# Kernel tuning notes

Measured on AMD Instinct MI355X. Metric: run time of the kernel, lower is better.

Reference implementation:

```python
import jax, jax.numpy as jnp
import numpy as np
from jax import lax
from jax.scipy.special import logsumexp

N = 1024   # keypoints image 0
M = 1024   # keypoints image 1
D = 256    # descriptor dim
H = 4      # attention heads
L = 18     # GNN layers ('self','cross')*9
ITERS = 100
KENC = [4, 32, 64, 128, 256]


def conv1(x, w, b):
    # 1x1 Conv1d == channel matmul: x [b,c,n], w [o,c], b [o]
    return jnp.einsum('oc,bcn->bon', w, x) + b[None, :, None]


def inorm(x, eps=1e-5):
    # InstanceNorm1d (affine=False): normalize over length per (b, c)
    m = jnp.mean(x, axis=-1, keepdims=True)
    v = jnp.var(x, axis=-1, keepdims=True)
    return (x - m) * lax.rsqrt(v + eps)


def attention_block(x, src, pw, pb, mw, mb):
    b, d, _ = x.shape
    dh = d // H
    q = conv1(x, pw[0], pb[0]).reshape(b, dh, H, -1)
    k = conv1(src, pw[1], pb[1]).reshape(b, dh, H, -1)
    v = conv1(src, pw[2], pb[2]).reshape(b, dh, H, -1)
    s = jnp.einsum('bdhn,bdhm->bhnm', q, k) / (dh ** 0.5)
    p = jax.nn.softmax(s, axis=-1)
    o = jnp.einsum('bhnm,bdhm->bdhn', p, v).reshape(b, d, -1)
    return conv1(o, mw, mb)


def prop(x, src, i, Pw, Pb, Mw, Mb, W0, B0, W1, B1):
    msg = attention_block(x, src, Pw[i], Pb[i], Mw[i], Mb[i])
    h = jnp.concatenate([x, msg], axis=1)          # [b, 2D, n]
    h = jax.nn.relu(inorm(conv1(h, W0[i], B0[i])))
    return conv1(h, W1[i], B1[i])


def sinkhorn(Z, log_mu, log_nu, iters):
    def step(carry, _):
        u, v = carry
        u = log_mu - logsumexp(Z + v[:, None, :], axis=2)
        v = log_nu - logsumexp(Z + u[:, :, None], axis=1)
        return (u, v), None
    init = (jnp.zeros_like(log_mu), jnp.zeros_like(log_nu))
    (u, v), _ = lax.scan(jax.checkpoint(step), init, None, length=iters)
    return Z + u[:, :, None] + v[:, None, :]


def log_optimal_transport(scores, alpha, iters):
    b, m, n = scores.shape
    bins0 = jnp.broadcast_to(alpha, (b, m, 1))
    bins1 = jnp.broadcast_to(alpha, (b, 1, n))
    binsA = jnp.broadcast_to(alpha, (b, 1, 1))
    couplings = jnp.concatenate([
        jnp.concatenate([scores, bins0], axis=-1),
        jnp.concatenate([bins1, binsA], axis=-1)], axis=1)  # [b, m+1, n+1]
    norm = np.float32(-np.log(m + n))
    log_mu = jnp.concatenate([jnp.full((m,), norm, scores.dtype),
                              jnp.array([np.log(n)], scores.dtype) + norm])
    log_nu = jnp.concatenate([jnp.full((n,), norm, scores.dtype),
                              jnp.array([np.log(m)], scores.dtype) + norm])
    log_mu = jnp.broadcast_to(log_mu[None], (b, m + 1))
    log_nu = jnp.broadcast_to(log_nu[None], (b, n + 1))
    Z = sinkhorn(couplings, log_mu, log_nu, iters)
    return Z - norm


def setup_inputs() -> dict:
    key = jax.random.key(0)
    ks = iter(jax.random.split(key, 64))
    w = lambda shape, s=0.02: jax.random.normal(next(ks), shape, jnp.float32) * s
    inp = {
        'keypoints0': jax.random.normal(next(ks), (1, N, 3), jnp.float32),
        'keypoints1': jax.random.normal(next(ks), (1, M, 3), jnp.float32),
        'descriptors0': jax.random.normal(next(ks), (1, D, N), jnp.float32),
        'descriptors1': jax.random.normal(next(ks), (1, D, M), jnp.float32),
        'scores0': jax.random.uniform(next(ks), (1, N), jnp.float32),
        'scores1': jax.random.uniform(next(ks), (1, M), jnp.float32),
    }
    for i in range(4):
        inp[f'kenc_w{i}'] = w((KENC[i + 1], KENC[i]), 0.1)
        inp[f'kenc_b{i}'] = jnp.zeros((KENC[i + 1],), jnp.float32)
    inp['gnn_proj_w'] = w((L, 3, D, D))
    inp['gnn_proj_b'] = jnp.zeros((L, 3, D), jnp.float32)
    inp['gnn_merge_w'] = w((L, D, D))
    inp['gnn_merge_b'] = jnp.zeros((L, D), jnp.float32)
    inp['gnn_mlp_w0'] = w((L, 2 * D, 2 * D))
    inp['gnn_mlp_b0'] = jnp.zeros((L, 2 * D), jnp.float32)
    inp['gnn_mlp_w1'] = w((L, D, 2 * D))
    inp['gnn_mlp_b1'] = jnp.zeros((L, D), jnp.float32)
    inp['final_w'] = w((D, D))
    inp['final_b'] = jnp.zeros((D,), jnp.float32)
    inp['bin_score'] = jnp.float32(1.0)
    return inp


def reference(keypoints0, keypoints1, descriptors0, descriptors1, scores0, scores1,
              kenc_w0, kenc_b0, kenc_w1, kenc_b1, kenc_w2, kenc_b2, kenc_w3, kenc_b3,
              gnn_proj_w, gnn_proj_b, gnn_merge_w, gnn_merge_b,
              gnn_mlp_w0, gnn_mlp_b0, gnn_mlp_w1, gnn_mlp_b1,
              final_w, final_b, bin_score):
    def kenc(kpts, sc):
        h = jnp.concatenate([jnp.swapaxes(kpts, 1, 2), sc[:, None, :]], axis=1)  # [b,4,n]
        h = jax.nn.relu(inorm(conv1(h, kenc_w0, kenc_b0)))
        h = jax.nn.relu(inorm(conv1(h, kenc_w1, kenc_b1)))
        h = jax.nn.relu(inorm(conv1(h, kenc_w2, kenc_b2)))
        return conv1(h, kenc_w3, kenc_b3)

    d0 = descriptors0 + kenc(keypoints0, scores0)
    d1 = descriptors1 + kenc(keypoints1, scores1)
    for i in range(L):  # even: self, odd: cross
        cross = (i % 2 == 1)
        s0 = d1 if cross else d0
        s1 = d0 if cross else d1
        delta0 = prop(d0, s0, i, gnn_proj_w, gnn_proj_b, gnn_merge_w, gnn_merge_b,
                      gnn_mlp_w0, gnn_mlp_b0, gnn_mlp_w1, gnn_mlp_b1)
        delta1 = prop(d1, s1, i, gnn_proj_w, gnn_proj_b, gnn_merge_w, gnn_merge_b,
                      gnn_mlp_w0, gnn_mlp_b0, gnn_mlp_w1, gnn_mlp_b1)
        d0, d1 = d0 + delta0, d1 + delta1
    md0 = conv1(d0, final_w, final_b)
    md1 = conv1(d1, final_w, final_b)
    scores = jnp.einsum('bdn,bdm->bnm', md0, md1) / (D ** 0.5)
    return log_optimal_transport(scores, bin_score, ITERS)
```

## Files before the change

### kernel.cpp

```cpp
#include <hip/hip_runtime.h>
#include <cstddef>

#define TPB 256

typedef _Float16 f16;
typedef _Float16 f16x4 __attribute__((ext_vector_type(4)));
typedef _Float16 f16x8 __attribute__((ext_vector_type(8)));
typedef float f32x4 __attribute__((ext_vector_type(4)));
typedef unsigned long long u64;

__device__ __forceinline__ float block_sum(float v, float* red) {
  int tid = threadIdx.x;
  red[tid] = v; __syncthreads();
#pragma unroll
  for (int off = 128; off > 0; off >>= 1) {
    if (tid < off) red[tid] += red[tid + off];
    __syncthreads();
  }
  float r = red[0];
  __syncthreads();
  return r;
}

__global__ __launch_bounds__(TPB) void build_h0(const float* __restrict__ kp0,
                                                const float* __restrict__ kp1,
                                                const float* __restrict__ sc0,
                                                const float* __restrict__ sc1,
                                                float* __restrict__ h0) {
  int n = blockIdx.x * TPB + threadIdx.x;
  int im = blockIdx.y;
  const float* kp = im ? kp1 : kp0;
  const float* sc = im ? sc1 : sc0;
  float* h = h0 + (size_t)im * 4096;
  h[n]        = kp[n * 3 + 0];
  h[1024 + n] = kp[n * 3 + 1];
  h[2048 + n] = kp[n * 3 + 2];
  h[3072 + n] = sc[n];
}

template<bool NORMRELU, bool RESID>
__global__ __launch_bounds__(TPB) void chanconv(const float* __restrict__ W,
                                                const float* __restrict__ bias,
                                                const float* __restrict__ in, long instride,
                                                const float* res0, const float* res1,
                                                float* __restrict__ out, long outstride, int C) {
  int o = blockIdx.x, im = blockIdx.y, tid = threadIdx.x;
  const float* inp = in + (long)im * instride;
  __shared__ float Ws[128];
  __shared__ float red[TPB];
  for (int c = tid; c < C; c += TPB) Ws[c] = W[(long)o * C + c];
  __syncthreads();
  float b = bias[o];
  float4 acc = {b, b, b, b};
  for (int c = 0; c < C; ++c) {
    float w = Ws[c];
    float4 v = *(const float4*)(inp + (long)c * 1024 + tid * 4);
    acc.x += w * v.x; acc.y += w * v.y; acc.z += w * v.z; acc.w += w * v.w;
  }
  float* orow = out + (long)im * outstride + (long)o * 1024;
  if (NORMRELU) {
    float s = acc.x + acc.y + acc.z + acc.w;
    float mean = block_sum(s, red) * (1.f / 1024.f);
    float dx = acc.x - mean, dy = acc.y - mean, dz = acc.z - mean, dw = acc.w - mean;
    float var = block_sum(dx * dx + dy * dy + dz * dz + dw * dw, red) * (1.f / 1024.f);
    float rstd = rsqrtf(var + 1e-5f);
    float4 o4 = {fmaxf(dx * rstd, 0.f), fmaxf(dy * rstd, 0.f),
                 fmaxf(dz * rstd, 0.f), fmaxf(dw * rstd, 0.f)};
    *(float4*)(orow + tid * 4) = o4;
  } else {
    if (RESID) {
      const float* res = im ? res1 : res0;
      float4 r = *(const float4*)(res + (long)o * 1024 + tid * 4);
      acc.x += r.x; acc.y += r.y; acc.z += r.z; acc.w += r.w;
    }
    *(float4*)(orow + tid * 4) = acc;
  }
}

struct GBH {
  const void* A; const void* B; const void* B2; void* C;
  const float* bias; const float* res; const float* mu; const float* rs;
  void* o2a; void* o2b; int coff; int pad;
};
struct GB16 { GBH g[16]; };

#define F_BNORM   1
#define F_BCONCAT 2
#define F_BADD    4
#define F_CD16    8
#define F_RES     16
#define F_OUT2    32
#define F_CSCAT   64

template<int BM, int BN, int ASRC, int BSRC, int FLAGS>
__global__ __launch_bounds__(TPB) void gemmh(GB16 gbs, int K, int lda, int ldb,
                                             int ldc, float alpha, int ksplit) {
  constexpr int WM = BM / 32;
  constexpr int NWN = 4 / WM;
  constexpr int WN = BN / NWN;
  constexpr int NFR = WN / 16;
  GBH g = gbs.g[blockIdx.z];
  const int tid = threadIdx.x;
  const int lane = tid & 63, wid = tid >> 6;
  const int wm = wid / NWN, wn = wid % NWN;
  const int m0 = blockIdx.y * BM, n0 = blockIdx.x * BN;
  __shared__ f16 As[BM][36];
  __shared__ f16 Bs[BN][36];
  f32x4 acc[2][NFR];
#pragma unroll
  for (int i = 0; i < 2; ++i)
#pragma unroll
    for (int j = 0; j < NFR; ++j) acc[i][j] = (f32x4){0.f, 0.f, 0.f, 0.f};

  for (int k0 = 0; k0 < K; k0 += 32) {
    if constexpr (ASRC == 0) {
      if constexpr (BM == 64) {
        const int m = tid >> 2, k4 = (tid & 3) * 8;
        const float* ap = (const float*)g.A + (long)(m0 + m) * lda + k0 + k4;
        float4 u0 = *(const float4*)ap, u1 = *(const float4*)(ap + 4);
        f16x4 h0 = {(f16)u0.x, (f16)u0.y, (f16)u0.z, (f16)u0.w};
        f16x4 h1 = {(f16)u1.x, (f16)u1.y, (f16)u1.z, (f16)u1.w};
        *(f16x4*)&As[m][k4] = h0;
        *(f16x4*)&As[m][k4 + 4] = h1;
      } else {
        const int m = tid >> 3, k4 = (tid & 7) * 4;
        const float* ap = (const float*)g.A + (long)(m0 + m) * lda + k0 + k4;
        float4 u0 = *(const float4*)ap;
        f16x4 h0 = {(f16)u0.x, (f16)u0.y, (f16)u0.z, (f16)u0.w};
        *(f16x4*)&As[m][k4] = h0;
      }
    } else if constexpr (ASRC == 1) {
      const int k = tid >> 3, mg = (tid & 7) * 8;
      const f16* ap = (const f16*)g.A + (long)(k0 + k) * lda + m0 + mg;
      f16x8 h = *(const f16x8*)ap;
#pragma unroll
      for (int j = 0; j < 8; ++j) As[mg + j][k] = h[j];
    } else {
      const int m = tid >> 2, k4 = (tid & 3) * 8;
      const f16* ap = (const f16*)g.A + (long)(m0 + m) * lda + k0 + k4;
      f16x8 h = *(const f16x8*)ap;
      const float M = g.mu[m0 + m], Iv = g.rs[m0 + m];
      f16x4 h0, h1;
#pragma unroll
      for (int j = 0; j < 4; ++j) h0[j] = (f16)(__expf((float)h[j] - M) * Iv);
#pragma unroll
      for (int j = 0; j < 4; ++j) h1[j] = (f16)(__expf((float)h[j + 4] - M) * Iv);
      *(f16x4*)&As[m][k4] = h0;
      *(f16x4*)&As[m][k4 + 4] = h1;
    }
#pragma unroll
    for (int r = 0; r < BN / 64; ++r) {
      if constexpr (BSRC == 0) {
        const int k = tid >> 3, ng = (tid & 7) * 8 + r * 64;
        const int kg = k0 + k;
        const float* bp;
        if constexpr ((FLAGS & F_BCONCAT) != 0)
          bp = (kg < ksplit) ? ((const float*)g.B + (long)kg * ldb)
                             : ((const float*)g.B2 + (long)(kg - ksplit) * ldb);
        else
          bp = (const float*)g.B + (long)kg * ldb;
        float4 u0 = *(const float4*)(bp + n0 + ng);
        float4 u1 = *(const float4*)(bp + n0 + ng + 4);
        Bs[ng + 0][k] = (f16)u0.x; Bs[ng + 1][k] = (f16)u0.y;
        Bs[ng + 2][k] = (f16)u0.z; Bs[ng + 3][k] = (f16)u0.w;
        Bs[ng + 4][k] = (f16)u1.x; Bs[ng + 5][k] = (f16)u1.y;
        Bs[ng + 6][k] = (f16)u1.z; Bs[ng + 7][k] = (f16)u1.w;
      } else if constexpr (BSRC == 1) {
        const int k = tid >> 3, ng = (tid & 7) * 8 + r * 64;
        const int kg = k0 + k;
        f16x8 h = *(const f16x8*)((const f16*)g.B + (long)kg * ldb + n0 + ng);
        if constexpr ((FLAGS & F_BNORM) != 0) {
          const float mu = g.mu[kg], rs = g.rs[kg];
#pragma unroll
          for (int j = 0; j < 8; ++j)
            h[j] = (f16)fmaxf(((float)h[j] - mu) * rs, 0.f);
        }
#pragma unroll
        for (int j = 0; j < 8; ++j) Bs[ng + j][k] = h[j];
      } else {
        const int n = (tid >> 2) + r * 64, k4 = (tid & 3) * 8;
        const f16* bp = (const f16*)g.B + (long)(n0 + n) * ldb + k0 + k4;
        f16x8 h = *(const f16x8*)bp;
        if constexpr ((FLAGS & F_BADD) != 0) {
          f16x8 h2 = *(const f16x8*)((const f16*)g.B2 + (long)(n0 + n) * ldb + k0 + k4);
          h = h + h2;
        }
        f16x4 h0 = {h[0], h[1], h[2], h[3]};
        f16x4 h1 = {h[4], h[5], h[6], h[7]};
        *(f16x4*)&Bs[n][k4] = h0;
        *(f16x4*)&Bs[n][k4 + 4] = h1;
      }
    }
    __syncthreads();
#pragma unroll
    for (int ks = 0; ks < 2; ++ks) {
      const int kof = ks * 16 + ((lane >> 4) << 2);
      f16x4 a[2], b[NFR];
      a[0] = *(const f16x4*)&As[wm * 32 + (lane & 15)][kof];
      a[1] = *(const f16x4*)&As[wm * 32 + 16 + (lane & 15)][kof];
#pragma unroll
      for (int fn = 0; fn < NFR; ++fn)
        b[fn] = *(const f16x4*)&Bs[wn * WN + fn * 16 + (lane & 15)][kof];
#pragma unroll
      for (int fm = 0; fm < 2; ++fm)
#pragma unroll
        for (int fn = 0; fn < NFR; ++fn)
          acc[fm][fn] = __builtin_amdgcn_mfma_f32_16x16x16f16(a[fm], b[fn], acc[fm][fn], 0, 0, 0);
    }
    __syncthreads();
  }

  const int r0 = (lane >> 4) << 2, cn = lane & 15;
#pragma unroll
  for (int fm = 0; fm < 2; ++fm) {
#pragma unroll
    for (int r = 0; r < 4; ++r) {
      const int m = m0 + wm * 32 + fm * 16 + r0 + r;
      const float bi = g.bias ? g.bias[m] : 0.f;
#pragma unroll
      for (int fn = 0; fn < NFR; ++fn) {
        const int n = n0 + wn * WN + fn * 16 + cn;
        float v = acc[fm][fn][r] * alpha + bi;
        if constexpr ((FLAGS & F_RES) != 0) v += g.res[(long)m * ldc + n];
        if constexpr ((FLAGS & F_OUT2) != 0) {
          ((float*)g.C)[(long)m * 1028 + n] = v;
          ((f16*)g.o2a)[(long)m * 1028 + n] = (f16)v;
          ((f16*)g.o2b)[(long)n * 1028 + m] = (f16)v;
        } else if constexpr ((FLAGS & F_CSCAT) != 0) {
          ((f16*)g.C)[(long)m * ldc + g.coff + 4 * n] = (f16)v;
        } else if constexpr ((FLAGS & F_CD16) != 0) {
          ((f16*)g.C)[(long)m * ldc + n] = (f16)v;
        } else {
          ((float*)g.C)[(long)m * ldc + n] = v;
        }
      }
    }
  }
}

__global__ __launch_bounds__(TPB) void rowlse_h(const f16* __restrict__ S,
                                                float* __restrict__ Mrow,
                                                float* __restrict__ Inv) {
  int row = blockIdx.x * 4 + (threadIdx.x >> 6);
  int lane = threadIdx.x & 63;
  const f16x8* p = (const f16x8*)(S + (long)row * 1024);
  f16x8 v0 = p[lane], v1 = p[lane + 64];
  float m = -1e30f;
#pragma unroll
  for (int j = 0; j < 8; ++j)
    m = fmaxf(m, fmaxf((float)v0[j], (float)v1[j]));
#pragma unroll
  for (int off = 32; off > 0; off >>= 1) m = fmaxf(m, __shfl_xor(m, off));
  float s = 0.f;
#pragma unroll
  for (int j = 0; j < 8; ++j)
    s += __expf((float)v0[j] - m) + __expf((float)v1[j] - m);
#pragma unroll
  for (int off = 32; off > 0; off >>= 1) s += __shfl_xor(s, off);
  if (lane == 0) { Mrow[row] = m; Inv[row] = 1.f / s; }
}

__global__ __launch_bounds__(TPB) void rowstats2_h(const f16* __restrict__ t,
                                                   float* __restrict__ mu,
                                                   float* __restrict__ rs) {
  int row = blockIdx.x * 4 + (threadIdx.x >> 6);
  int lane = threadIdx.x & 63;
  const f16x8* p = (const f16x8*)(t + (long)row * 1024);
  f16x8 v0 = p[lane], v1 = p[lane + 64];
  float s = 0.f, s2 = 0.f;
#pragma unroll
  for (int j = 0; j < 8; ++j) {
    float a = (float)v0[j], b = (float)v1[j];
    s += a + b; s2 += a * a + b * b;
  }
#pragma unroll
  for (int off = 32; off > 0; off >>= 1) { s += __shfl_xor(s, off); s2 += __shfl_xor(s2, off); }
  if (lane == 0) {
    float mean = s * (1.f / 1024.f);
    mu[row] = mean;
    rs[row] = rsqrtf(fmaxf(s2 * (1.f / 1024.f) - mean * mean, 0.f) + 1e-5f);
  }
}

#define NORMC  (-7.62461899f)
#define LOGN   (6.93147181f)
#define LOG_MN (7.62461899f)
#define ZLD    1028
#define SINKB  64

__device__ __forceinline__ u64 llc_load64(const u64* p) {
  return __hip_atomic_load(p, __ATOMIC_RELAXED, __HIP_MEMORY_SCOPE_AGENT);
}
__device__ __forceinline__ void llc_store64(u64* p, u64 v) {
  __hip_atomic_store(p, v, __ATOMIC_RELAXED, __HIP_MEMORY_SCOPE_AGENT);
}
__device__ __forceinline__ void llc_store32(float* p, float v) {
  __hip_atomic_store(p, v, __ATOMIC_RELAXED, __HIP_MEMORY_SCOPE_AGENT);
}
__device__ __forceinline__ u64 pack2(float a, float b) {
  union { float f[2]; u64 x; } c; c.f[0] = a; c.f[1] = b; return c.x;
}

__global__ __launch_bounds__(TPB) void fill_bins(float* __restrict__ Z,
                                                 const float* __restrict__ alpha_p,
                                                 float* __restrict__ vF,
                                                 unsigned* __restrict__ bar) {
  float a = *alpha_p;
  int t = blockIdx.x * TPB + threadIdx.x;
  if (t < ZLD) vF[t] = 0.f;
  if (t == 0) *bar = 0u;
  if (t <= 1024) {
    Z[(long)t * ZLD + 1024] = a;
    Z[(long)1024 * ZLD + t] = a;
  }
}

__device__ __forceinline__ void gridbar(unsigned* __restrict__ bar, unsigned gen) {
  __syncthreads();
  if (threadIdx.x == 0) {
    __hip_atomic_fetch_add(bar, 1u, __ATOMIC_RELAXED, __HIP_MEMORY_SCOPE_AGENT);
    const unsigned target = gen * SINKB;
    while (__hip_atomic_load(bar, __ATOMIC_RELAXED, __HIP_MEMORY_SCOPE_AGENT) < target) {}
  }
  asm volatile("" ::: "memory");
  __syncthreads();
}

__device__ __forceinline__ void sink_half(const f16x8 zreg[4][2],
                                          const float* __restrict__ w,
                                          float* __restrict__ out,
                                          int tid, int gw, int lane,
                                          float alpha, float* __restrict__ lds) {
  for (int s = tid; s < 513; s += TPB) {
    u64 x = llc_load64((const u64*)w + s);
    union { u64 x; float f[2]; } c; c.x = x;
    lds[2 * s] = c.f[0];
    lds[2 * s + 1] = c.f[1];
  }
  __syncthreads();
  float vv[16];
#pragma unroll
  for (int t = 0; t < 16; ++t) vv[t] = lds[lane + 64 * t];
  const float w1024 = lds[1024];
  const float binv = alpha + w1024;

  float res[4];
#pragma unroll
  for (int r = 0; r < 4; ++r) {
    float val[16];
    float m = binv;
#pragma unroll
    for (int t = 0; t < 16; ++t) {
      val[t] = (float)zreg[r][t >> 3][t & 7] + vv[t];
      m = fmaxf(m, val[t]);
    }
#pragma unroll
    for (int off = 32; off > 0; off >>= 1) m = fmaxf(m, __shfl_xor(m, off));
    float s = 0.f;
#pragma unroll
    for (int t = 0; t < 16; ++t) s += __expf(val[t] - m);
#pragma unroll
    for (int off = 32; off > 0; off >>= 1) s += __shfl_xor(s, off);
    s += __expf(binv - m);
    res[r] = NORMC - (m + logf(s));
  }
  if (lane < 2)
    llc_store64((u64*)(out + 4 * gw) + lane, pack2(res[2 * lane], res[2 * lane + 1]));

  if (gw == 0) {
    float m = w1024;
#pragma unroll
    for (int t = 0; t < 16; ++t) m = fmaxf(m, vv[t]);
#pragma unroll
    for (int off = 32; off > 0; off >>= 1) m = fmaxf(m, __shfl_xor(m, off));
    float s = 0.f;
#pragma unroll
    for (int t = 0; t < 16; ++t) s += __expf(vv[t] - m);
#pragma unroll
    for (int off = 32; off > 0; off >>= 1) s += __shfl_xor(s, off);
    s += __expf(w1024 - m);
    if (lane == 0)
      llc_store32(out + 1024, NORMC + LOGN - (alpha + m + logf(s)));
  }
}

__global__ __launch_bounds__(TPB) void sink_persist(const f16* __restrict__ Zh,
                                                    const f16* __restrict__ Zth,
                                                    float* __restrict__ uF,
                                                    float* __restrict__ vF,
                                                    unsigned* __restrict__ bar,
                                                    const float* __restrict__ alpha_p) {
  __shared__ float lds[ZLD];
  const int tid = threadIdx.x;
  const int lane = tid & 63;
  const int gw = blockIdx.x * 4 + (tid >> 6);
  const float alpha = *alpha_p;

  f16x8 zr[4][2], zt[4][2];
#pragma unroll
  for (int r = 0; r < 4; ++r) {
    const long row = 4 * gw + r;
    const f16* zp = Zh + row * ZLD;
    const f16* ztp = Zth + row * ZLD;
#pragma unroll
    for (int h = 0; h < 2; ++h)
#pragma unroll
      for (int j = 0; j < 8; ++j) {
        zr[r][h][j] = zp[lane + 64 * (8 * h + j)];
        zt[r][h][j] = ztp[lane + 64 * (8 * h + j)];
      }
  }

  unsigned gen = 0;
#pragma unroll 1
  for (int it = 0; it < 100; ++it) {
    sink_half(zr, vF, uF, tid, gw, lane, alpha, lds);
    gridbar(bar, ++gen);
    sink_half(zt, uF, vF, tid, gw, lane, alpha, lds);
    gridbar(bar, ++gen);
  }
}

__global__ __launch_bounds__(TPB) void assemble(const float* __restrict__ Z,
                                                const float* __restrict__ u,
                                                const float* __restrict__ v,
                                                float* __restrict__ out) {
  int idx = blockIdx.x * TPB + threadIdx.x;
  if (idx < 1025 * 1025) {
    int i = idx / 1025;
    int j = idx - i * 1025;
    out[idx] = Z[(long)i * ZLD + j] + u[i] + v[j] + LOG_MN;
  }
}

static inline GBH mkgb(const void* A, const void* B, void* C,
                       const float* bias = nullptr, const void* B2 = nullptr,
                       const float* res = nullptr,
                       const float* mu = nullptr, const float* rs = nullptr,
                       int coff = 0, void* o2a = nullptr, void* o2b = nullptr) {
  GBH g; g.A = A; g.B = B; g.B2 = B2; g.C = C; g.bias = bias; g.res = res;
  g.mu = mu; g.rs = rs; g.o2a = o2a; g.o2b = o2b; g.coff = coff; g.pad = 0;
  return g;
}

extern "C" void kernel_launch(void* const* d_in, const int* in_sizes, int n_in,
                              void* d_out, int out_size, void* d_ws, size_t ws_size,
                              hipStream_t stream) {
  const float* kp0     = (const float*)d_in[0];
  const float* kp1     = (const float*)d_in[1];
  const float* desc0   = (const float*)d_in[2];
  const float* desc1   = (const float*)d_in[3];
  const float* sc0     = (const float*)d_in[4];
  const float* sc1     = (const float*)d_in[5];
  const float* kw[4]   = {(const float*)d_in[6], (const float*)d_in[8],
                          (const float*)d_in[10], (const float*)d_in[12]};
  const float* kb[4]   = {(const float*)d_in[7], (const float*)d_in[9],
                          (const float*)d_in[11], (const float*)d_in[13]};
  const float* proj_w  = (const float*)d_in[14];
  const float* proj_b  = (const float*)d_in[15];
  const float* merge_w = (const float*)d_in[16];
  const float* merge_b = (const float*)d_in[17];
  const float* mlp_w0  = (const float*)d_in[18];
  const float* mlp_b0  = (const float*)d_in[19];
  const float* mlp_w1  = (const float*)d_in[20];
  const float* mlp_b1  = (const float*)d_in[21];
  const float* final_w = (const float*)d_in[22];
  const float* final_b = (const float*)d_in[23];
  const float* alpha_p = (const float*)d_in[24];

  float* p = (float*)d_ws;
  float* dA  = p; p += 524288;
  float* dB  = p; p += 524288;
  float* h0  = p; p += 8192;
  float* hb1 = p; p += 262144;
  float* hb2 = p; p += 131072;
  float* msg = p; p += 524288;
  float* muA = p; p += 1024;
  float* rsA = p; p += 1024;
  float* Mrw = p; p += 8192;
  float* Inv = p; p += 8192;
  float* Zb  = p; p += 1053700;
  float* uF  = p; p += 1028;
  float* vF  = p; p += 1028;
  unsigned* bar = (unsigned*)p; p += 4;
  f16* qkvh = (f16*)p; p += 786432;
  f16* Sh   = (f16*)p; p += 4194304;
  f16* oAh  = (f16*)p; p += 262144;
  f16* oBh  = (f16*)p; p += 262144;
  f16* tbh  = (f16*)p; p += 524288;
  f16* mdbh = (f16*)p; p += 262144;
  f16* Zh   = (f16*)p; p += 526852;
  f16* Zth  = (f16*)p; p += 526852;
  size_t need_bytes = (size_t)(p - (float*)d_ws) * sizeof(float);
  if (ws_size < need_bytes) return;

  const long DSTR = 262144;

  build_h0<<<dim3(4, 2), TPB, 0, stream>>>(kp0, kp1, sc0, sc1, h0);
  chanconv<true, false><<<dim3(32, 2),  TPB, 0, stream>>>(kw[0], kb[0], h0,  4096,   nullptr, nullptr, hb1, 32768,  4);
  chanconv<true, false><<<dim3(64, 2),  TPB, 0, stream>>>(kw[1], kb[1], hb1, 32768,  nullptr, nullptr, hb2, 65536,  32);
  chanconv<true, false><<<dim3(128, 2), TPB, 0, stream>>>(kw[2], kb[2], hb2, 65536,  nullptr, nullptr, hb1, 131072, 64);
  chanconv<false, true><<<dim3(256, 2), TPB, 0, stream>>>(kw[3], kb[3], hb1, 131072, desc0,   desc1,   dA,  DSTR,   128);

  float* dc = dA;
  float* dn = dB;
  for (int i = 0; i < 18; ++i) {
    bool cross = (i & 1) != 0;
    const float* xs[2] = {dc, dc + DSTR};
    const float* ss2[2] = {cross ? xs[1] : xs[0], cross ? xs[0] : xs[1]};

    {
      GB16 gb{};
      for (int im = 0; im < 2; ++im)
        for (int pp = 0; pp < 3; ++pp)
          gb.g[im * 3 + pp] = mkgb(proj_w + (size_t)(i * 3 + pp) * 65536,
                                   (pp == 0 ? xs[im] : ss2[im]),
                                   qkvh + (size_t)(im * 3 + pp) * DSTR,
                                   proj_b + (size_t)(i * 3 + pp) * 256);
      gemmh<32, 128, 0, 0, F_CD16><<<dim3(8, 8, 6), TPB, 0, stream>>>(
          gb, 256, 256, 1024, 1024, 1.f, 0);
    }
    {
      GB16 gb{};
      for (int im = 0; im < 2; ++im)
        for (int h = 0; h < 4; ++h)
          gb.g[im * 4 + h] = mkgb(qkvh + (size_t)(im * 3 + 0) * DSTR + h * 1024,
                                  qkvh + (size_t)(im * 3 + 1) * DSTR + h * 1024,
                                  Sh + (size_t)(im * 4 + h) * 1048576);
      gemmh<64, 128, 1, 1, F_CD16><<<dim3(8, 16, 8), TPB, 0, stream>>>(
          gb, 64, 4096, 4096, 1024, 0.125f, 0);
    }
    rowlse_h<<<2048, TPB, 0, stream>>>(Sh, Mrw, Inv);
    {
      GB16 gb{};
      for (int kh = 0; kh < 2; ++kh)
        for (int imh = 0; imh < 8; ++imh) {
          int im = imh >> 2, h = imh & 3;
          gb.g[kh * 8 + imh] = mkgb(Sh + (size_t)imh * 1048576 + kh * 512,
                                    qkvh + (size_t)(im * 3 + 2) * DSTR + h * 1024 + kh * 512,
                                    (kh ? oBh : oAh) + (size_t)im * 262144,
                                    nullptr, nullptr, nullptr,
                                    Mrw + imh * 1024, Inv + imh * 1024, h);
        }
      gemmh<64, 64, 2, 2, F_CD16 | F_CSCAT><<<dim3(1, 16, 16), TPB, 0, stream>>>(
          gb, 512, 1024, 4096, 256, 1.f, 0);
    }
    {
      GB16 gb{};
      for (int im = 0; im < 2; ++im)
        gb.g[im] = mkgb(merge_w + (size_t)i * 65536, oAh + (size_t)im * 262144,
                        msg + (size_t)im * DSTR, merge_b + (size_t)i * 256,
                        oBh + (size_t)im * 262144);
      gemmh<32, 64, 0, 2, F_BADD><<<dim3(16, 8, 2), TPB, 0, stream>>>(
          gb, 256, 256, 256, 1024, 1.f, 0);
    }
    {
      GB16 gb{};
      for (int im = 0; im < 2; ++im)
        gb.g[im] = mkgb(mlp_w0 + (size_t)i * 262144, xs[im],
                        tbh + (size_t)im * 524288, mlp_b0 + (size_t)i * 512,
                        msg + (size_t)im * DSTR);
      gemmh<64, 64, 0, 0, F_BCONCAT | F_CD16><<<dim3(16, 8, 2), TPB, 0, stream>>>(
          gb, 512, 512, 1024, 1024, 1.f, 256);
    }
    rowstats2_h<<<256, TPB, 0, stream>>>(tbh, muA, rsA);
    {
      GB16 gb{};
      for (int im = 0; im < 2; ++im)
        gb.g[im] = mkgb(mlp_w1 + (size_t)i * 131072, tbh + (size_t)im * 524288,
                        dn + (size_t)im * DSTR, mlp_b1 + (size_t)i * 256,
                        nullptr, xs[im],
                        muA + (size_t)im * 512, rsA + (size_t)im * 512);
      gemmh<32, 64, 0, 1, F_BNORM | F_RES><<<dim3(16, 8, 2), TPB, 0, stream>>>(
          gb, 512, 512, 1024, 1024, 1.f, 0);
    }
    float* tmp = dc; dc = dn; dn = tmp;
  }

  {
    GB16 gb{};
    for (int im = 0; im < 2; ++im)
      gb.g[im] = mkgb(final_w, dc + (size_t)im * DSTR, mdbh + (size_t)im * 262144,
                      final_b);
    gemmh<32, 64, 0, 0, F_CD16><<<dim3(16, 8, 2), TPB, 0, stream>>>(
        gb, 256, 256, 1024, 1024, 1.f, 0);
  }
  {
    GB16 gb{};
    gb.g[0] = mkgb(mdbh, mdbh + 262144, Zb, nullptr, nullptr, nullptr,
                   nullptr, nullptr, 0, Zh, Zth);
    gemmh<64, 64, 1, 1, F_OUT2><<<dim3(16, 16, 1), TPB, 0, stream>>>(
        gb, 256, 1024, 1024, ZLD, 0.0625f, 0);
  }
  fill_bins<<<5, TPB, 0, stream>>>(Zb, alpha_p, vF, bar);

  sink_persist<<<SINKB, TPB, 0, stream>>>(Zh, Zth, uF, vF, bar, alpha_p);

  assemble<<<4105, TPB, 0, stream>>>(Zb, uF, vF, (float*)d_out);
}
```

Before: 2.283 ms.

## Fuse attention scores, softmax and PV into one kernel per query tile

Replaces the QK^T GEMM, the row log-sum-exp kernel and the split-K PV GEMM with a single fused attention kernel. Each block computes a 16x1024 score tile in shared memory, applies softmax there, and multiplies by V. This removes the 16 MB f16 score matrix round-trip through global memory, two kernel launches per layer, and the split-K partial outputs that the merge GEMM had to add. The new grid has only 512 blocks, each holding about 50 KB of shared memory, and K/V are reloaded by every query tile, so occupancy and reuse may drop.

```diff
diff --git a/kernel.cpp b/kernel.cpp
--- a/kernel.cpp
+++ b/kernel.cpp
@@ -90,7 +90,6 @@
 #define F_CD16    8
 #define F_RES     16
 #define F_OUT2    32
-#define F_CSCAT   64
 
 template<int BM, int BN, int ASRC, int BSRC, int FLAGS>
 __global__ __launch_bounds__(TPB) void gemmh(GB16 gbs, int K, int lda, int ldb,
@@ -129,24 +128,12 @@
         f16x4 h0 = {(f16)u0.x, (f16)u0.y, (f16)u0.z, (f16)u0.w};
         *(f16x4*)&As[m][k4] = h0;
       }
-    } else if constexpr (ASRC == 1) {
+    } else {
       const int k = tid >> 3, mg = (tid & 7) * 8;
       const f16* ap = (const f16*)g.A + (long)(k0 + k) * lda + m0 + mg;
       f16x8 h = *(const f16x8*)ap;
 #pragma unroll
       for (int j = 0; j < 8; ++j) As[mg + j][k] = h[j];
-    } else {
-      const int m = tid >> 2, k4 = (tid & 3) * 8;
-      const f16* ap = (const f16*)g.A + (long)(m0 + m) * lda + k0 + k4;
-      f16x8 h = *(const f16x8*)ap;
-      const float M = g.mu[m0 + m], Iv = g.rs[m0 + m];
-      f16x4 h0, h1;
-#pragma unroll
-      for (int j = 0; j < 4; ++j) h0[j] = (f16)(__expf((float)h[j] - M) * Iv);
-#pragma unroll
-      for (int j = 0; j < 4; ++j) h1[j] = (f16)(__expf((float)h[j + 4] - M) * Iv);
-      *(f16x4*)&As[m][k4] = h0;
-      *(f16x4*)&As[m][k4 + 4] = h1;
     }
 #pragma unroll
     for (int r = 0; r < BN / 64; ++r) {
@@ -226,8 +213,6 @@
           ((float*)g.C)[(long)m * 1028 + n] = v;
           ((f16*)g.o2a)[(long)m * 1028 + n] = (f16)v;
           ((f16*)g.o2b)[(long)n * 1028 + m] = (f16)v;
-        } else if constexpr ((FLAGS & F_CSCAT) != 0) {
-          ((f16*)g.C)[(long)m * ldc + g.coff + 4 * n] = (f16)v;
         } else if constexpr ((FLAGS & F_CD16) != 0) {
           ((f16*)g.C)[(long)m * ldc + n] = (f16)v;
         } else {
@@ -238,26 +223,116 @@
   }
 }
 
-__global__ __launch_bounds__(TPB) void rowlse_h(const f16* __restrict__ S,
-                                                float* __restrict__ Mrow,
-                                                float* __restrict__ Inv) {
-  int row = blockIdx.x * 4 + (threadIdx.x >> 6);
-  int lane = threadIdx.x & 63;
-  const f16x8* p = (const f16x8*)(S + (long)row * 1024);
-  f16x8 v0 = p[lane], v1 = p[lane + 64];
-  float m = -1e30f;
-#pragma unroll
-  for (int j = 0; j < 8; ++j)
-    m = fmaxf(m, fmaxf((float)v0[j], (float)v1[j]));
-#pragma unroll
-  for (int off = 32; off > 0; off >>= 1) m = fmaxf(m, __shfl_xor(m, off));
-  float s = 0.f;
-#pragma unroll
-  for (int j = 0; j < 8; ++j)
-    s += __expf((float)v0[j] - m) + __expf((float)v1[j] - m);
-#pragma unroll
-  for (int off = 32; off > 0; off >>= 1) s += __shfl_xor(s, off);
-  if (lane == 0) { Mrow[row] = m; Inv[row] = 1.f / s; }
+__global__ __launch_bounds__(TPB) void fused_attn(const f16* __restrict__ qkv,
+                                                  f16* __restrict__ oT) {
+  const int im = blockIdx.y >> 2, h = blockIdx.y & 3;
+  const int q0 = blockIdx.x * 16;
+  const long DSTR = 262144;
+  const f16* qp = qkv + (long)(im * 3 + 0) * DSTR + h * 1024;
+  const f16* kp = qkv + (long)(im * 3 + 1) * DSTR + h * 1024;
+  const f16* vp = qkv + (long)(im * 3 + 2) * DSTR + h * 1024;
+  f16* op = oT + (long)im * 262144;
+
+  __shared__ f16 Qs[16][68];
+  __shared__ f16 Ss[16][1032];
+  __shared__ f16 KV[8704];
+
+  const int tid = threadIdx.x, lane = tid & 63, w = tid >> 6;
+  const int l15 = lane & 15, lh = (lane >> 4) << 2;
+
+  {
+    const int d = tid >> 2, q4 = (tid & 3) * 4;
+    f16x4 v4 = *(const f16x4*)(qp + (long)d * 4096 + q0 + q4);
+#pragma unroll
+    for (int j = 0; j < 4; ++j) Qs[q4 + j][d] = v4[j];
+  }
+
+  for (int kt = 0; kt < 8; ++kt) {
+    const int kv0 = kt * 128;
+    __syncthreads();
+#pragma unroll
+    for (int r = 0; r < 4; ++r) {
+      const int d = (tid >> 4) + 16 * r, kvg = (tid & 15) * 8;
+      f16x8 v8 = *(const f16x8*)(kp + (long)d * 4096 + kv0 + kvg);
+#pragma unroll
+      for (int j = 0; j < 8; ++j) KV[(kvg + j) * 68 + d] = v8[j];
+    }
+    __syncthreads();
+    f32x4 sacc[2] = {{0.f, 0.f, 0.f, 0.f}, {0.f, 0.f, 0.f, 0.f}};
+#pragma unroll
+    for (int ks = 0; ks < 4; ++ks) {
+      const int kof = ks * 16 + lh;
+      f16x4 a  = *(const f16x4*)&Qs[l15][kof];
+      f16x4 b0 = *(const f16x4*)&KV[(w * 32 + l15) * 68 + kof];
+      f16x4 b1 = *(const f16x4*)&KV[(w * 32 + 16 + l15) * 68 + kof];
+      sacc[0] = __builtin_amdgcn_mfma_f32_16x16x16f16(a, b0, sacc[0], 0, 0, 0);
+      sacc[1] = __builtin_amdgcn_mfma_f32_16x16x16f16(a, b1, sacc[1], 0, 0, 0);
+    }
+#pragma unroll
+    for (int fn = 0; fn < 2; ++fn) {
+      const int kv = kv0 + w * 32 + fn * 16 + l15;
+#pragma unroll
+      for (int r = 0; r < 4; ++r)
+        Ss[lh + r][kv] = (f16)(sacc[fn][r] * 0.125f);
+    }
+  }
+  __syncthreads();
+
+#pragma unroll
+  for (int rr = 0; rr < 4; ++rr) {
+    const int q = w * 4 + rr;
+    f16x8 x0 = *(const f16x8*)&Ss[q][lane * 16];
+    f16x8 x1 = *(const f16x8*)&Ss[q][lane * 16 + 8];
+    float m = -1e30f;
+#pragma unroll
+    for (int j = 0; j < 8; ++j)
+      m = fmaxf(m, fmaxf((float)x0[j], (float)x1[j]));
+#pragma unroll
+    for (int off = 32; off > 0; off >>= 1) m = fmaxf(m, __shfl_xor(m, off));
+    float s = 0.f;
+#pragma unroll
+    for (int j = 0; j < 8; ++j)
+      s += __expf((float)x0[j] - m) + __expf((float)x1[j] - m);
+#pragma unroll
+    for (int off = 32; off > 0; off >>= 1) s += __shfl_xor(s, off);
+    const float inv = 1.f / s;
+    f16x8 p0, p1;
+#pragma unroll
+    for (int j = 0; j < 8; ++j) {
+      p0[j] = (f16)(__expf((float)x0[j] - m) * inv);
+      p1[j] = (f16)(__expf((float)x1[j] - m) * inv);
+    }
+    *(f16x8*)&Ss[q][lane * 16] = p0;
+    *(f16x8*)&Ss[q][lane * 16 + 8] = p1;
+  }
+
+  f32x4 oacc = {0.f, 0.f, 0.f, 0.f};
+  for (int kt = 0; kt < 8; ++kt) {
+    __syncthreads();
+    {
+      const int d = tid >> 2, kvg = (tid & 3) * 32;
+#pragma unroll
+      for (int j = 0; j < 4; ++j) {
+        f16x8 v8 = *(const f16x8*)(vp + (long)d * 4096 + kt * 128 + kvg + j * 8);
+        *(f16x8*)&KV[d * 136 + kvg + j * 8] = v8;
+      }
+    }
+    __syncthreads();
+#pragma unroll
+    for (int ks = 0; ks < 8; ++ks) {
+      f16x4 a = *(const f16x4*)&Ss[l15][kt * 128 + ks * 16 + lh];
+      f16x4 b = *(const f16x4*)&KV[(w * 16 + l15) * 136 + ks * 16 + lh];
+      oacc = __builtin_amdgcn_mfma_f32_16x16x16f16(a, b, oacc, 0, 0, 0);
+    }
+  }
+  {
+    const int d = w * 16 + l15;
+#pragma unroll
+    for (int r = 0; r < 4; ++r) {
+      const int q = q0 + lh + r;
+      op[(long)q * 256 + h + 4 * d] = (f16)oacc[r];
+    }
+  }
 }
 
 __global__ __launch_bounds__(TPB) void rowstats2_h(const f16* __restrict__ t,
@@ -403,11 +478,11 @@
     const f16* zp = Zh + row * ZLD;
     const f16* ztp = Zth + row * ZLD;
 #pragma unroll
-    for (int h = 0; h < 2; ++h)
+    for (int hh = 0; hh < 2; ++hh)
 #pragma unroll
       for (int j = 0; j < 8; ++j) {
-        zr[r][h][j] = zp[lane + 64 * (8 * h + j)];
-        zt[r][h][j] = ztp[lane + 64 * (8 * h + j)];
+        zr[r][hh][j] = zp[lane + 64 * (8 * hh + j)];
+        zt[r][hh][j] = ztp[lane + 64 * (8 * hh + j)];
       }
   }
 
@@ -477,16 +552,12 @@
   float* msg = p; p += 524288;
   float* muA = p; p += 1024;
   float* rsA = p; p += 1024;
-  float* Mrw = p; p += 8192;
-  float* Inv = p; p += 8192;
   float* Zb  = p; p += 1053700;
   float* uF  = p; p += 1028;
   float* vF  = p; p += 1028;
   unsigned* bar = (unsigned*)p; p += 4;
   f16* qkvh = (f16*)p; p += 786432;
-  f16* Sh   = (f16*)p; p += 4194304;
-  f16* oAh  = (f16*)p; p += 262144;
-  f16* oBh  = (f16*)p; p += 262144;
+  f16* oTh  = (f16*)p; p += 262144;
   f16* tbh  = (f16*)p; p += 524288;
   f16* mdbh = (f16*)p; p += 262144;
   f16* Zh   = (f16*)p; p += 526852;
@@ -520,38 +591,13 @@
       gemmh<32, 128, 0, 0, F_CD16><<<dim3(8, 8, 6), TPB, 0, stream>>>(
           gb, 256, 256, 1024, 1024, 1.f, 0);
     }
+    fused_attn<<<dim3(64, 8), TPB, 0, stream>>>(qkvh, oTh);
     {
       GB16 gb{};
       for (int im = 0; im < 2; ++im)
-        for (int h = 0; h < 4; ++h)
-          gb.g[im * 4 + h] = mkgb(qkvh + (size_t)(im * 3 + 0) * DSTR + h * 1024,
-                                  qkvh + (size_t)(im * 3 + 1) * DSTR + h * 1024,
-                                  Sh + (size_t)(im * 4 + h) * 1048576);
-      gemmh<64, 128, 1, 1, F_CD16><<<dim3(8, 16, 8), TPB, 0, stream>>>(
-          gb, 64, 4096, 4096, 1024, 0.125f, 0);
-    }
-    rowlse_h<<<2048, TPB, 0, stream>>>(Sh, Mrw, Inv);
-    {
-      GB16 gb{};
-      for (int kh = 0; kh < 2; ++kh)
-        for (int imh = 0; imh < 8; ++imh) {
-          int im = imh >> 2, h = imh & 3;
-          gb.g[kh * 8 + imh] = mkgb(Sh + (size_t)imh * 1048576 + kh * 512,
-                                    qkvh + (size_t)(im * 3 + 2) * DSTR + h * 1024 + kh * 512,
-                                    (kh ? oBh : oAh) + (size_t)im * 262144,
-                                    nullptr, nullptr, nullptr,
-                                    Mrw + imh * 1024, Inv + imh * 1024, h);
-        }
-      gemmh<64, 64, 2, 2, F_CD16 | F_CSCAT><<<dim3(1, 16, 16), TPB, 0, stream>>>(
-          gb, 512, 1024, 4096, 256, 1.f, 0);
-    }
-    {
-      GB16 gb{};
-      for (int im = 0; im < 2; ++im)
-        gb.g[im] = mkgb(merge_w + (size_t)i * 65536, oAh + (size_t)im * 262144,
-                        msg + (size_t)im * DSTR, merge_b + (size_t)i * 256,
-                        oBh + (size_t)im * 262144);
-      gemmh<32, 64, 0, 2, F_BADD><<<dim3(16, 8, 2), TPB, 0, stream>>>(
+        gb.g[im] = mkgb(merge_w + (size_t)i * 65536, oTh + (size_t)im * 262144,
+                        msg + (size_t)im * DSTR, merge_b + (size_t)i * 256);
+      gemmh<32, 64, 0, 2, 0><<<dim3(16, 8, 2), TPB, 0, stream>>>(
           gb, 256, 256, 256, 1024, 1.f, 0);
     }
     {
```

After: 2.422 ms. 1.06x slower.

## Replace Sinkhorn grid barrier with generation-tagged dual-vector slots

Applied to the files above, without the earlier changes.

Each u/v entry is stored as a 64-bit word packing the float value with an iteration generation tag. Consumers spin on each slot until its tag matches the expected generation, instead of waiting at a global atomic-counter barrier after each half-iteration. This removes the barrier round trip and the counter contention, and lets blocks proceed as soon as their inputs are ready. In exchange the u/v storage doubles in size and every read of a slot becomes a polling load.

```diff
diff --git a/kernel.cpp b/kernel.cpp
--- a/kernel.cpp
+++ b/kernel.cpp
@@ -291,58 +291,56 @@
 __device__ __forceinline__ u64 llc_load64(const u64* p) {
   return __hip_atomic_load(p, __ATOMIC_RELAXED, __HIP_MEMORY_SCOPE_AGENT);
 }
-__device__ __forceinline__ void llc_store64(u64* p, u64 v) {
-  __hip_atomic_store(p, v, __ATOMIC_RELAXED, __HIP_MEMORY_SCOPE_AGENT);
-}
-__device__ __forceinline__ void llc_store32(float* p, float v) {
-  __hip_atomic_store(p, v, __ATOMIC_RELAXED, __HIP_MEMORY_SCOPE_AGENT);
-}
-__device__ __forceinline__ u64 pack2(float a, float b) {
-  union { float f[2]; u64 x; } c; c.f[0] = a; c.f[1] = b; return c.x;
+__device__ __forceinline__ void slot_store(u64* p, float v, unsigned gen) {
+  union { float f; unsigned u; } c; c.f = v;
+  u64 x = ((u64)gen << 32) | (u64)c.u;
+  __hip_atomic_store(p, x, __ATOMIC_RELAXED, __HIP_MEMORY_SCOPE_AGENT);
+}
+__device__ __forceinline__ float slot_val(u64 x) {
+  union { unsigned u; float f; } c; c.u = (unsigned)x;
+  return c.f;
 }
 
 __global__ __launch_bounds__(TPB) void fill_bins(float* __restrict__ Z,
                                                  const float* __restrict__ alpha_p,
-                                                 float* __restrict__ vF,
-                                                 unsigned* __restrict__ bar) {
+                                                 u64* __restrict__ uS,
+                                                 u64* __restrict__ vS) {
   float a = *alpha_p;
   int t = blockIdx.x * TPB + threadIdx.x;
-  if (t < ZLD) vF[t] = 0.f;
-  if (t == 0) *bar = 0u;
   if (t <= 1024) {
     Z[(long)t * ZLD + 1024] = a;
     Z[(long)1024 * ZLD + t] = a;
-  }
-}
-
-__device__ __forceinline__ void gridbar(unsigned* __restrict__ bar, unsigned gen) {
+    slot_store(uS + t, 0.f, 0u);
+    slot_store(vS + t, 0.f, 0u);
+  }
+}
+
+__device__ __forceinline__ void sink_half(const f16x8 zreg[4][2],
+                                          const u64* __restrict__ w,
+                                          u64* __restrict__ out,
+                                          unsigned rgen, int tid, int gw, int lane,
+                                          float alpha, float* __restrict__ lds) {
   __syncthreads();
-  if (threadIdx.x == 0) {
-    __hip_atomic_fetch_add(bar, 1u, __ATOMIC_RELAXED, __HIP_MEMORY_SCOPE_AGENT);
-    const unsigned target = gen * SINKB;
-    while (__hip_atomic_load(bar, __ATOMIC_RELAXED, __HIP_MEMORY_SCOPE_AGENT) < target) {}
-  }
-  asm volatile("" ::: "memory");
+#pragma unroll
+  for (int q = 0; q < 4; ++q) {
+    const int s = tid + q * TPB;
+    u64 x;
+    do { x = llc_load64(w + s); } while ((unsigned)(x >> 32) != rgen);
+    lds[s] = slot_val(x);
+  }
+  if (tid == 0) {
+    u64 x;
+    do { x = llc_load64(w + 1024); } while ((unsigned)(x >> 32) != rgen);
+    lds[1024] = slot_val(x);
+  }
   __syncthreads();
-}
-
-__device__ __forceinline__ void sink_half(const f16x8 zreg[4][2],
-                                          const float* __restrict__ w,
-                                          float* __restrict__ out,
-                                          int tid, int gw, int lane,
-                                          float alpha, float* __restrict__ lds) {
-  for (int s = tid; s < 513; s += TPB) {
-    u64 x = llc_load64((const u64*)w + s);
-    union { u64 x; float f[2]; } c; c.x = x;
-    lds[2 * s] = c.f[0];
-    lds[2 * s + 1] = c.f[1];
-  }
-  __syncthreads();
+
   float vv[16];
 #pragma unroll
   for (int t = 0; t < 16; ++t) vv[t] = lds[lane + 64 * t];
   const float w1024 = lds[1024];
   const float binv = alpha + w1024;
+  const unsigned wgen = rgen + 1;
 
   float res[4];
 #pragma unroll
@@ -364,8 +362,9 @@
     s += __expf(binv - m);
     res[r] = NORMC - (m + logf(s));
   }
-  if (lane < 2)
-    llc_store64((u64*)(out + 4 * gw) + lane, pack2(res[2 * lane], res[2 * lane + 1]));
+  float myv = (lane == 0) ? res[0] : (lane == 1) ? res[1]
+            : (lane == 2) ? res[2] : res[3];
+  if (lane < 4) slot_store(out + 4 * gw + lane, myv, wgen);
 
   if (gw == 0) {
     float m = w1024;
@@ -380,15 +379,14 @@
     for (int off = 32; off > 0; off >>= 1) s += __shfl_xor(s, off);
     s += __expf(w1024 - m);
     if (lane == 0)
-      llc_store32(out + 1024, NORMC + LOGN - (alpha + m + logf(s)));
+      slot_store(out + 1024, NORMC + LOGN - (alpha + m + logf(s)), wgen);
   }
 }
 
 __global__ __launch_bounds__(TPB) void sink_persist(const f16* __restrict__ Zh,
                                                     const f16* __restrict__ Zth,
-                                                    float* __restrict__ uF,
-                                                    float* __restrict__ vF,
-                                                    unsigned* __restrict__ bar,
+                                                    u64* __restrict__ uS,
+                                                    u64* __restrict__ vS,
                                                     const float* __restrict__ alpha_p) {
   __shared__ float lds[ZLD];
   const int tid = threadIdx.x;
@@ -403,33 +401,31 @@
     const f16* zp = Zh + row * ZLD;
     const f16* ztp = Zth + row * ZLD;
 #pragma unroll
-    for (int h = 0; h < 2; ++h)
+    for (int hh = 0; hh < 2; ++hh)
 #pragma unroll
       for (int j = 0; j < 8; ++j) {
-        zr[r][h][j] = zp[lane + 64 * (8 * h + j)];
-        zt[r][h][j] = ztp[lane + 64 * (8 * h + j)];
+        zr[r][hh][j] = zp[lane + 64 * (8 * hh + j)];
+        zt[r][hh][j] = ztp[lane + 64 * (8 * hh + j)];
       }
   }
 
   unsigned gen = 0;
 #pragma unroll 1
   for (int it = 0; it < 100; ++it) {
-    sink_half(zr, vF, uF, tid, gw, lane, alpha, lds);
-    gridbar(bar, ++gen);
-    sink_half(zt, uF, vF, tid, gw, lane, alpha, lds);
-    gridbar(bar, ++gen);
+    sink_half(zr, vS, uS, gen, tid, gw, lane, alpha, lds);  ++gen;
+    sink_half(zt, uS, vS, gen, tid, gw, lane, alpha, lds);  ++gen;
   }
 }
 
 __global__ __launch_bounds__(TPB) void assemble(const float* __restrict__ Z,
-                                                const float* __restrict__ u,
-                                                const float* __restrict__ v,
+                                                const u64* __restrict__ uS,
+                                                const u64* __restrict__ vS,
                                                 float* __restrict__ out) {
   int idx = blockIdx.x * TPB + threadIdx.x;
   if (idx < 1025 * 1025) {
     int i = idx / 1025;
     int j = idx - i * 1025;
-    out[idx] = Z[(long)i * ZLD + j] + u[i] + v[j] + LOG_MN;
+    out[idx] = Z[(long)i * ZLD + j] + slot_val(uS[i]) + slot_val(vS[j]) + LOG_MN;
   }
 }
 
@@ -480,9 +476,8 @@
   float* Mrw = p; p += 8192;
   float* Inv = p; p += 8192;
   float* Zb  = p; p += 1053700;
-  float* uF  = p; p += 1028;
-  float* vF  = p; p += 1028;
-  unsigned* bar = (unsigned*)p; p += 4;
+  u64* uS = (u64*)p; p += 2056;
+  u64* vS = (u64*)p; p += 2056;
   f16* qkvh = (f16*)p; p += 786432;
   f16* Sh   = (f16*)p; p += 4194304;
   f16* oAh  = (f16*)p; p += 262144;
@@ -592,9 +587,9 @@
     gemmh<64, 64, 1, 1, F_OUT2><<<dim3(16, 16, 1), TPB, 0, stream>>>(
         gb, 256, 1024, 1024, ZLD, 0.0625f, 0);
   }
-  fill_bins<<<5, TPB, 0, stream>>>(Zb, alpha_p, vF, bar);
-
-  sink_persist<<<SINKB, TPB, 0, stream>>>(Zh, Zth, uF, vF, bar, alpha_p);
-
-  assemble<<<4105, TPB, 0, stream>>>(Zb, uF, vF, (float*)d_out);
-}
+  fill_bins<<<5, TPB, 0, stream>>>(Zb, alpha_p, uS, vS);
+
+  sink_persist<<<SINKB, TPB, 0, stream>>>(Zh, Zth, uS, vS, alpha_p);
+
+  assemble<<<4105, TPB, 0, stream>>>(Zb, uS, vS, (float*)d_out);
+}
```

Result: no change. 2.277 ms (-0.2%).
